# Optimization experiments

Hardware: AMD Instinct MI355X
Metric: run time of the kernel (lower is better)

The kernel has to match this reference:

```python
import jax, jax.numpy as jnp
import numpy as np

NEG_SLOPE = 0.2  # PyG GATConv default negative_slope


def gat_conv(x, edge_index, W, att_src, att_dst, b, num_nodes):
    """PyG-style GATConv: lin -> edge attention (LeakyReLU) -> segment softmax
    over destination nodes -> scatter-add aggregation. Self-loops added
    (PyG default add_self_loops=True). Heads concatenated."""
    H, C = att_src.shape
    h = (x @ W).reshape(num_nodes, H, C)            # [N, H, C]
    # add self loops
    loops = jnp.arange(num_nodes, dtype=edge_index.dtype)
    src = jnp.concatenate([edge_index[0], loops])   # [E+N]
    dst = jnp.concatenate([edge_index[1], loops])
    a_src = jnp.einsum('nhc,hc->nh', h, att_src)    # [N, H]
    a_dst = jnp.einsum('nhc,hc->nh', h, att_dst)
    alpha = a_src[src] + a_dst[dst]                 # [E+N, H]
    alpha = jnp.where(alpha > 0, alpha, NEG_SLOPE * alpha)  # LeakyReLU
    # numerically stable segment softmax over destination nodes
    amax = jax.lax.stop_gradient(
        jax.ops.segment_max(alpha, dst, num_segments=num_nodes))
    e = jnp.exp(alpha - amax[dst])
    denom = jax.ops.segment_sum(e, dst, num_segments=num_nodes)
    w = e / denom[dst]                              # [E+N, H]
    msg = h[src] * w[:, :, None]                    # [E+N, H, C]
    out = jax.ops.segment_sum(msg, dst, num_segments=num_nodes)  # [N, H, C]
    return out.reshape(num_nodes, H * C) + b


def setup_inputs() -> dict:
    key = jax.random.key(0)
    ks = jax.random.split(key, 12)
    N1, N2, E1, E2 = 50000, 10000, 800000, 160000
    IN, OUT, H = 256, 32, 4
    s = 0.1
    return {
        'x1': jax.random.normal(ks[0], (N1, IN), dtype=jnp.float32),
        'edge_index1': jax.random.randint(ks[1], (2, E1), 0, N1, dtype=jnp.int64),
        'x2': jax.random.normal(ks[2], (N2, IN), dtype=jnp.float32),
        'edge_index2': jax.random.randint(ks[3], (2, E2), 0, N2, dtype=jnp.int64),
        'group_assignment': jax.random.randint(ks[4], (N1,), 0, N2, dtype=jnp.int64),
        'W1': jax.random.normal(ks[5], (IN, H * OUT), dtype=jnp.float32) * s,
        'att_src1': jax.random.normal(ks[6], (H, OUT), dtype=jnp.float32) * s,
        'att_dst1': jax.random.normal(ks[7], (H, OUT), dtype=jnp.float32) * s,
        'b1': jnp.zeros((H * OUT,), dtype=jnp.float32),
        'W2': jax.random.normal(ks[8], (IN, H * OUT), dtype=jnp.float32) * s,
        'att_src2': jax.random.normal(ks[9], (H, OUT), dtype=jnp.float32) * s,
        'att_dst2': jax.random.normal(ks[10], (H, OUT), dtype=jnp.float32) * s,
        'b2': jnp.zeros((H * OUT,), dtype=jnp.float32),
    }


def reference(x1, edge_index1, x2, edge_index2, group_assignment,
              W1, att_src1, att_dst1, b1, W2, att_src2, att_dst2, b2):
    x1_out = gat_conv(x1, edge_index1, W1, att_src1, att_dst1, b1, x1.shape[0])
    x2_out = gat_conv(x2, edge_index2, W2, att_src2, att_dst2, b2, x2.shape[0])
    x1_combined = x1_out + x2_out[group_assignment]
    return (x1_combined, x2_out)
```

## Files before the change

### kernel.cpp

```cpp
#include <hip/hip_runtime.h>
#include <hip/hip_bf16.h>
#include <string.h>

#define IN_DIM 256
#define HC 128
#define HH 4
#define NEG_SLOPE 0.2f
#define BKT 64
#define NBMAX 1024
#define CAPB 2048

typedef __attribute__((ext_vector_type(8))) short bf16x8;
typedef __attribute__((ext_vector_type(4))) float f32x4;

__device__ __forceinline__ unsigned short f2b(float f) {
    __hip_bfloat16 h = __float2bfloat16(f);
    unsigned short u;
    memcpy(&u, &h, 2);
    return u;
}
__device__ __forceinline__ unsigned int pk2(float a, float b) {
    float2 t; t.x = a; t.y = b;
    __hip_bfloat162 p = __float22bfloat162_rn(t);
    unsigned int u;
    memcpy(&u, &p, 4);
    return u;
}
__device__ __forceinline__ bf16x8 cvt8(const float4 lo, const float4 hi) {
    union { unsigned int u[4]; bf16x8 v; } r;
    r.u[0] = pk2(lo.x, lo.y); r.u[1] = pk2(lo.z, lo.w);
    r.u[2] = pk2(hi.x, hi.y); r.u[3] = pk2(hi.z, hi.w);
    return r.v;
}
__device__ __forceinline__ float b2f(unsigned short u) {
    return __uint_as_float(((unsigned int)u) << 16);
}

__global__ void prep_kernel(const float* __restrict__ W1, const float* __restrict__ W2,
                            unsigned short* __restrict__ Wt1, unsigned short* __restrict__ Wt2) {
    const float* W = blockIdx.x ? W2 : W1;
    unsigned short* Wt = blockIdx.x ? Wt2 : Wt1;
    for (int idx = threadIdx.x; idx < HC * IN_DIM; idx += 256) {
        int c = idx >> 8, k = idx & 255;
        Wt[idx] = f2b(W[k * HC + c]);
    }
}

__device__ __forceinline__ void gemm_body(int blk, int tid,
                                          const float* __restrict__ x,
                                          const unsigned short* __restrict__ Wt,
                                          const float* __restrict__ attS,
                                          const float* __restrict__ attD,
                                          unsigned short* __restrict__ hb,
                                          float* __restrict__ asrc,
                                          float* __restrict__ adst, int N) {
    const int lane = tid & 63;
    const int wid = tid >> 6;
    const int lr = lane & 15, lg = lane >> 4;
    const int r0 = blk * 128 + wid * 32;
    int ra0 = r0 + lr;      if (ra0 > N - 1) ra0 = N - 1;
    int ra1 = r0 + 16 + lr; if (ra1 > N - 1) ra1 = N - 1;
    const float* A0 = x + (size_t)ra0 * IN_DIM + lg * 8;
    const float* A1 = x + (size_t)ra1 * IN_DIM + lg * 8;
    const unsigned short* B0 = Wt + (size_t)lr * IN_DIM + lg * 8;

    f32x4 acc[2][8];
#pragma unroll
    for (int h = 0; h < 2; ++h)
#pragma unroll
        for (int t = 0; t < 8; ++t) acc[h][t] = (f32x4){0.f, 0.f, 0.f, 0.f};

#pragma unroll
    for (int k0 = 0; k0 < IN_DIM; k0 += 32) {
        float4 a0l = *(const float4*)(A0 + k0);
        float4 a0h = *(const float4*)(A0 + k0 + 4);
        float4 a1l = *(const float4*)(A1 + k0);
        float4 a1h = *(const float4*)(A1 + k0 + 4);
        bf16x8 a0 = cvt8(a0l, a0h);
        bf16x8 a1 = cvt8(a1l, a1h);
#pragma unroll
        for (int t = 0; t < 8; ++t) {
            bf16x8 b = *(const bf16x8*)(B0 + t * 16 * IN_DIM + k0);
            acc[0][t] = __builtin_amdgcn_mfma_f32_16x16x32_bf16(a0, b, acc[0][t], 0, 0, 0);
            acc[1][t] = __builtin_amdgcn_mfma_f32_16x16x32_bf16(a1, b, acc[1][t], 0, 0, 0);
        }
    }

    float attS_r[8], attD_r[8];
#pragma unroll
    for (int t = 0; t < 8; ++t) {
        attS_r[t] = attS[t * 16 + lr];
        attD_r[t] = attD[t * 16 + lr];
    }

#pragma unroll
    for (int half = 0; half < 2; ++half) {
#pragma unroll
        for (int i = 0; i < 4; ++i) {
            int row = r0 + half * 16 + 4 * lg + i;
            float s[4] = {0.f, 0.f, 0.f, 0.f}, dd[4] = {0.f, 0.f, 0.f, 0.f};
#pragma unroll
            for (int t = 0; t < 8; ++t) {
                float c = acc[half][t][i];
                s[t >> 1] += c * attS_r[t];
                dd[t >> 1] += c * attD_r[t];
            }
#pragma unroll
            for (int m = 1; m < 16; m <<= 1) {
#pragma unroll
                for (int h = 0; h < 4; ++h) {
                    s[h] += __shfl_xor(s[h], m);
                    dd[h] += __shfl_xor(dd[h], m);
                }
            }
            if (row < N) {
#pragma unroll
                for (int t = 0; t < 8; ++t)
                    hb[(size_t)row * HC + t * 16 + lr] = f2b(acc[half][t][i]);
                if (lr == 0) {
#pragma unroll
                    for (int h = 0; h < 4; ++h) {
                        asrc[row * HH + h] = s[h];
                        adst[row * HH + h] = dd[h];
                    }
                }
            }
        }
    }
}

__launch_bounds__(256)
__global__ void mega_kernel(const float* __restrict__ x1,
                            const unsigned short* __restrict__ Wt1,
                            const float* __restrict__ attS1, const float* __restrict__ attD1,
                            unsigned short* __restrict__ hb1,
                            float* __restrict__ asrc1, float* __restrict__ adst1, int N1,
                            const float* __restrict__ x2,
                            const unsigned short* __restrict__ Wt2,
                            const float* __restrict__ attS2, const float* __restrict__ attD2,
                            unsigned short* __restrict__ hb2,
                            float* __restrict__ asrc2, float* __restrict__ adst2, int N2,
                            int G1) {
    const int b = blockIdx.x;
    const int tid = threadIdx.x;
    if (b < G1) gemm_body(b, tid, x1, Wt1, attS1, attD1, hb1, asrc1, adst1, N1);
    else        gemm_body(b - G1, tid, x2, Wt2, attS2, attD2, hb2, asrc2, adst2, N2);
}

__launch_bounds__(512)
__global__ void pass2_kernel(const int* __restrict__ ei1, int E1, int S1,
                             const int* __restrict__ ei2, int E2, int S2,
                             int nb1, int nbtot,
                             int* __restrict__ gcursor, int* __restrict__ rec) {
    __shared__ int hcnt[NBMAX];
    __shared__ int hoff[NBMAX];
    const int tid = threadIdx.x;
    for (int t = tid; t < NBMAX; t += 512) hcnt[t] = 0;
    __syncthreads();
    const int ebase = blockIdx.x * 4096;
    int myb[8], lrank[8], myrec[8];
#pragma unroll
    for (int k = 0; k < 8; ++k) {
        int i = ebase + tid + k * 512;
        int bkt = -1, src = 0, dstl = 0;
        if (i < S1) {
            int s, d;
            if (i < E1) { s = ei1[i]; d = ei1[E1 + i]; } else { s = d = i - E1; }
            bkt = d >> 6; src = s; dstl = d & 63;
        } else if (i < S1 + S2) {
            int q = i - S1, s, d;
            if (q < E2) { s = ei2[q]; d = ei2[E2 + q]; } else { s = d = q - E2; }
            bkt = nb1 + (d >> 6); src = s; dstl = d & 63;
        }
        myb[k] = bkt;
        myrec[k] = src | (dstl << 26);
        lrank[k] = (bkt >= 0) ? atomicAdd(&hcnt[bkt], 1) : 0;
    }
    __syncthreads();
    for (int t = tid; t < nbtot; t += 512)
        if (hcnt[t]) hoff[t] = atomicAdd(&gcursor[t], hcnt[t]);
    __syncthreads();
#pragma unroll
    for (int k = 0; k < 8; ++k) {
        int bkt = myb[k];
        if (bkt >= 0) {
            int pos = hoff[bkt] + lrank[k];
            if (pos < CAPB) rec[(size_t)bkt * CAPB + pos] = myrec[k];
        }
    }
}

__launch_bounds__(512)
__global__ void pass3_kernel(const int* __restrict__ rec, const int* __restrict__ gcursor,
                             int boff,
                             const unsigned short* __restrict__ hp,
                             const float* __restrict__ asrc, const float* __restrict__ adst,
                             const float* __restrict__ bias,
                             const int* __restrict__ ga,
                             const float* __restrict__ other,
                             float* __restrict__ out, int N) {
    __shared__ int srec[CAPB + 16];
    __shared__ int ncnt[BKT];
    __shared__ int nsc[BKT];
    __shared__ int ncur[BKT];
    __shared__ float adl[BKT * HH];
    const int tid = threadIdx.x;
    const int B = boff + blockIdx.x;
    const int n0 = blockIdx.x * BKT;
    int mycnt = gcursor[B];
    if (mycnt > CAPB) mycnt = CAPB;
    const int base = B * CAPB;

    for (int t = tid; t < BKT * HH; t += 512) {
        int node = n0 + (t >> 2);
        adl[t] = (node < N) ? adst[node * HH + (t & 3)] : 0.f;
    }
    if (tid < BKT) { ncnt[tid] = 0; ncur[tid] = 0; }
    __syncthreads();
    for (int t = tid; t < mycnt; t += 512) {
        int r = rec[base + t];
        atomicAdd(&ncnt[(r >> 26) & 63], 1);
    }
    __syncthreads();
    if (tid < 64) {
        int v = ncnt[tid];
#pragma unroll
        for (int off = 1; off < 64; off <<= 1) {
            int u = __shfl_up(v, off);
            if (tid >= off) v += u;
        }
        nsc[tid] = v;
    }
    if (tid < 16) srec[mycnt + tid] = 0;
    __syncthreads();
    for (int t = tid; t < mycnt; t += 512) {
        int r = rec[base + t];
        int dl = (r >> 26) & 63;
        int pos = nsc[dl] - ncnt[dl] + atomicAdd(&ncur[dl], 1);
        srec[pos] = r;
    }
    __syncthreads();

    const int slot = tid >> 5;
    const int j = tid & 31;
    const int head = j >> 3;
    const unsigned short* hbj = hp + 4 * j;

#pragma unroll
    for (int nl = 0; nl < 4; ++nl) {
        const int nloc = slot + (nl << 4);
        const int len = ncnt[nloc];
        float4 acc = {0.f, 0.f, 0.f, 0.f};
        float ws = 0.f;
        if (len > 0) {
            const int s0 = nsc[nloc] - len;
            const float adv = adl[nloc * HH + head];
            int rC[4], rN[4];
            float aC[4];
            ushort4 hC[4];
#pragma unroll
            for (int k = 0; k < 4; ++k) rC[k] = srec[s0 + k];
#pragma unroll
            for (int k = 0; k < 4; ++k) {
                int s = rC[k] & 0x3FFFFFF;
                aC[k] = asrc[s * HH + head];
                hC[k] = *(const ushort4*)(hbj + (size_t)s * HC);
            }
#pragma unroll
            for (int k = 0; k < 4; ++k) rN[k] = srec[s0 + 4 + k];
            for (int e = 0; e < len; e += 4) {
#pragma unroll
                for (int k = 0; k < 4; ++k) {
                    float alpha = aC[k] + adv;
                    alpha = alpha > 0.f ? alpha : NEG_SLOPE * alpha;
                    float w = (e + k < len) ? __expf(alpha) : 0.f;
                    acc.x += w * b2f(hC[k].x);
                    acc.y += w * b2f(hC[k].y);
                    acc.z += w * b2f(hC[k].z);
                    acc.w += w * b2f(hC[k].w);
                    ws += w;
                }
#pragma unroll
                for (int k = 0; k < 4; ++k) rC[k] = rN[k];
#pragma unroll
                for (int k = 0; k < 4; ++k) {
                    int s = rC[k] & 0x3FFFFFF;
                    aC[k] = asrc[s * HH + head];
                    hC[k] = *(const ushort4*)(hbj + (size_t)s * HC);
                }
#pragma unroll
                for (int k = 0; k < 4; ++k) rN[k] = srec[s0 + e + 8 + k];
            }
        }
        int node = n0 + nloc;
        if (node < N) {
            float inv = 1.f / ws;
            const float4 bb = *(const float4*)(bias + 4 * j);
            float4 o = {acc.x * inv + bb.x, acc.y * inv + bb.y,
                        acc.z * inv + bb.z, acc.w * inv + bb.w};
            if (ga) {
                const float4 ov = *(const float4*)(other + (size_t)ga[node] * HC + 4 * j);
                o.x += ov.x; o.y += ov.y; o.z += ov.z; o.w += ov.w;
            }
            *(float4*)(out + (size_t)node * HC + 4 * j) = o;
        }
    }
}

extern "C" void kernel_launch(void* const* d_in, const int* in_sizes, int n_in,
                              void* d_out, int out_size, void* d_ws, size_t ws_size,
                              hipStream_t stream) {
    const float* x1  = (const float*)d_in[0];
    const int*   ei1 = (const int*)d_in[1];
    const float* x2  = (const float*)d_in[2];
    const int*   ei2 = (const int*)d_in[3];
    const int*   ga  = (const int*)d_in[4];
    const float* W1    = (const float*)d_in[5];
    const float* attS1 = (const float*)d_in[6];
    const float* attD1 = (const float*)d_in[7];
    const float* b1    = (const float*)d_in[8];
    const float* W2    = (const float*)d_in[9];
    const float* attS2 = (const float*)d_in[10];
    const float* attD2 = (const float*)d_in[11];
    const float* b2    = (const float*)d_in[12];

    const int N1 = in_sizes[0] / IN_DIM;
    const int E1 = in_sizes[1] / 2;
    const int N2 = in_sizes[2] / IN_DIM;
    const int E2 = in_sizes[3] / 2;
    const int S1 = E1 + N1, S2 = E2 + N2;
    const int nb1 = (N1 + BKT - 1) / BKT;
    const int nb2 = (N2 + BKT - 1) / BKT;
    const int nbtot = nb1 + nb2;

    char* p = (char*)d_ws;
    auto alloc = [&](size_t bytes) {
        char* r = p; p += (bytes + 511) & ~(size_t)511; return r;
    };
    unsigned short* hb1 = (unsigned short*)alloc((size_t)N1 * HC * 2);
    unsigned short* hb2 = (unsigned short*)alloc((size_t)N2 * HC * 2);
    unsigned short* Wt1 = (unsigned short*)alloc((size_t)IN_DIM * HC * 2);
    unsigned short* Wt2 = (unsigned short*)alloc((size_t)IN_DIM * HC * 2);
    float* asrc1 = (float*)alloc((size_t)N1 * HH * 4);
    float* adst1 = (float*)alloc((size_t)N1 * HH * 4);
    float* asrc2 = (float*)alloc((size_t)N2 * HH * 4);
    float* adst2 = (float*)alloc((size_t)N2 * HH * 4);
    int* gcursor = (int*)alloc(NBMAX * 4);
    int* rec     = (int*)alloc((size_t)nbtot * CAPB * 4);

    float* out1 = (float*)d_out;
    float* out2 = (float*)d_out + (size_t)N1 * HC;

    (void)hipMemsetAsync(gcursor, 0, NBMAX * 4, stream);

    prep_kernel<<<2, 256, 0, stream>>>(W1, W2, Wt1, Wt2);

    const int G1 = (N1 + 127) / 128, G2 = (N2 + 127) / 128;
    mega_kernel<<<G1 + G2, 256, 0, stream>>>(
        x1, Wt1, attS1, attD1, hb1, asrc1, adst1, N1,
        x2, Wt2, attS2, attD2, hb2, asrc2, adst2, N2, G1);

    const int GP = (S1 + S2 + 4095) / 4096;
    pass2_kernel<<<GP, 512, 0, stream>>>(ei1, E1, S1, ei2, E2, S2,
                                         nb1, nbtot, gcursor, rec);

    pass3_kernel<<<nb2, 512, 0, stream>>>(rec, gcursor, nb1, hb2, asrc2, adst2,
                                          b2, nullptr, nullptr, out2, N2);
    pass3_kernel<<<nb1, 512, 0, stream>>>(rec, gcursor, 0, hb1, asrc1, adst1,
                                          b1, ga, out2, out1, N1);
}
```

Before: 130.2 us.

## Store h head-major and precompute bf16 edge weights in LDS for aggregation

The GEMM now writes projected features in a head-major layout ([H][N][32]), so each head's gather touches a 64-byte row. The aggregation kernel precomputes the exp(LeakyReLU) attention weights once per edge into a shared bf16 array, then processes one head at a time. Within each head, four edges are handled in parallel across lane groups, with a shuffle reduction at the end. This aims to cut redundant asrc loads and exp work and to shorten gathered rows, but it adds an extra LDS pass, rounds the weights to bf16, and runs four serial head loops per node.

```diff
diff --git a/kernel.cpp b/kernel.cpp
--- a/kernel.cpp
+++ b/kernel.cpp
@@ -51,7 +51,7 @@
                                           const unsigned short* __restrict__ Wt,
                                           const float* __restrict__ attS,
                                           const float* __restrict__ attD,
-                                          unsigned short* __restrict__ hb,
+                                          unsigned short* __restrict__ hq,
                                           float* __restrict__ asrc,
                                           float* __restrict__ adst, int N) {
     const int lane = tid & 63;
@@ -116,7 +116,8 @@
             if (row < N) {
 #pragma unroll
                 for (int t = 0; t < 8; ++t)
-                    hb[(size_t)row * HC + t * 16 + lr] = f2b(acc[half][t][i]);
+                    hq[((size_t)(t >> 1) * N + row) * 32 + (t & 1) * 16 + lr] =
+                        f2b(acc[half][t][i]);
                 if (lr == 0) {
 #pragma unroll
                     for (int h = 0; h < 4; ++h) {
@@ -133,18 +134,18 @@
 __global__ void mega_kernel(const float* __restrict__ x1,
                             const unsigned short* __restrict__ Wt1,
                             const float* __restrict__ attS1, const float* __restrict__ attD1,
-                            unsigned short* __restrict__ hb1,
+                            unsigned short* __restrict__ hq1,
                             float* __restrict__ asrc1, float* __restrict__ adst1, int N1,
                             const float* __restrict__ x2,
                             const unsigned short* __restrict__ Wt2,
                             const float* __restrict__ attS2, const float* __restrict__ attD2,
-                            unsigned short* __restrict__ hb2,
+                            unsigned short* __restrict__ hq2,
                             float* __restrict__ asrc2, float* __restrict__ adst2, int N2,
                             int G1) {
     const int b = blockIdx.x;
     const int tid = threadIdx.x;
-    if (b < G1) gemm_body(b, tid, x1, Wt1, attS1, attD1, hb1, asrc1, adst1, N1);
-    else        gemm_body(b - G1, tid, x2, Wt2, attS2, attD2, hb2, asrc2, adst2, N2);
+    if (b < G1) gemm_body(b, tid, x1, Wt1, attS1, attD1, hq1, asrc1, adst1, N1);
+    else        gemm_body(b - G1, tid, x2, Wt2, attS2, attD2, hq2, asrc2, adst2, N2);
 }
 
 __launch_bounds__(512)
@@ -193,13 +194,14 @@
 __launch_bounds__(512)
 __global__ void pass3_kernel(const int* __restrict__ rec, const int* __restrict__ gcursor,
                              int boff,
-                             const unsigned short* __restrict__ hp,
+                             const unsigned short* __restrict__ hq,
                              const float* __restrict__ asrc, const float* __restrict__ adst,
                              const float* __restrict__ bias,
                              const int* __restrict__ ga,
                              const float* __restrict__ other,
                              float* __restrict__ out, int N) {
     __shared__ int srec[CAPB + 16];
+    __shared__ unsigned short wrec[(CAPB + 16) * HH];
     __shared__ int ncnt[BKT];
     __shared__ int nsc[BKT];
     __shared__ int ncur[BKT];
@@ -217,10 +219,8 @@
     }
     if (tid < BKT) { ncnt[tid] = 0; ncur[tid] = 0; }
     __syncthreads();
-    for (int t = tid; t < mycnt; t += 512) {
-        int r = rec[base + t];
-        atomicAdd(&ncnt[(r >> 26) & 63], 1);
-    }
+    for (int t = tid; t < mycnt; t += 512)
+        atomicAdd(&ncnt[(rec[base + t] >> 26) & 63], 1);
     __syncthreads();
     if (tid < 64) {
         int v = ncnt[tid];
@@ -231,7 +231,11 @@
         }
         nsc[tid] = v;
     }
-    if (tid < 16) srec[mycnt + tid] = 0;
+    if (tid < 16) {
+        srec[mycnt + tid] = 0;
+#pragma unroll
+        for (int h = 0; h < HH; ++h) wrec[(mycnt + tid) * HH + h] = 0;
+    }
     __syncthreads();
     for (int t = tid; t < mycnt; t += 512) {
         int r = rec[base + t];
@@ -240,69 +244,77 @@
         srec[pos] = r;
     }
     __syncthreads();
+    for (int t = tid; t < mycnt; t += 512) {
+        int r = srec[t];
+        int s = r & 0x3FFFFFF;
+        int dl = (r >> 26) & 63;
+        const float4 a = *(const float4*)(asrc + (size_t)s * HH);
+        float al[4] = {a.x + adl[dl * HH + 0], a.y + adl[dl * HH + 1],
+                       a.z + adl[dl * HH + 2], a.w + adl[dl * HH + 3]};
+#pragma unroll
+        for (int h = 0; h < HH; ++h) {
+            float v = al[h];
+            v = v > 0.f ? v : NEG_SLOPE * v;
+            wrec[t * HH + h] = f2b(__expf(v));
+        }
+    }
+    __syncthreads();
 
     const int slot = tid >> 5;
     const int j = tid & 31;
-    const int head = j >> 3;
-    const unsigned short* hbj = hp + 4 * j;
+    const int g = j >> 3;
+    const int cj = j & 7;
 
 #pragma unroll
     for (int nl = 0; nl < 4; ++nl) {
         const int nloc = slot + (nl << 4);
         const int len = ncnt[nloc];
-        float4 acc = {0.f, 0.f, 0.f, 0.f};
-        float ws = 0.f;
-        if (len > 0) {
-            const int s0 = nsc[nloc] - len;
-            const float adv = adl[nloc * HH + head];
-            int rC[4], rN[4];
-            float aC[4];
-            ushort4 hC[4];
-#pragma unroll
-            for (int k = 0; k < 4; ++k) rC[k] = srec[s0 + k];
-#pragma unroll
-            for (int k = 0; k < 4; ++k) {
-                int s = rC[k] & 0x3FFFFFF;
-                aC[k] = asrc[s * HH + head];
-                hC[k] = *(const ushort4*)(hbj + (size_t)s * HC);
-            }
-#pragma unroll
-            for (int k = 0; k < 4; ++k) rN[k] = srec[s0 + 4 + k];
+        const int s0 = nsc[nloc] - len;
+        const int node = n0 + nloc;
+        int gnode = 0;
+        if (ga && node < N) gnode = ga[node];
+#pragma unroll
+        for (int h = 0; h < HH; ++h) {
+            const unsigned short* hqh = hq + (size_t)h * N * 32 + cj * 4;
+            float4 acc = {0.f, 0.f, 0.f, 0.f};
+            float ws = 0.f;
+            int idx = s0 + g;
+            float w = (g < len) ? b2f(wrec[idx * HH + h]) : 0.f;
+            int s = srec[idx] & 0x3FFFFFF;
+            ushort4 hv = *(const ushort4*)(hqh + (size_t)s * 32);
             for (int e = 0; e < len; e += 4) {
-#pragma unroll
-                for (int k = 0; k < 4; ++k) {
-                    float alpha = aC[k] + adv;
-                    alpha = alpha > 0.f ? alpha : NEG_SLOPE * alpha;
-                    float w = (e + k < len) ? __expf(alpha) : 0.f;
-                    acc.x += w * b2f(hC[k].x);
-                    acc.y += w * b2f(hC[k].y);
-                    acc.z += w * b2f(hC[k].z);
-                    acc.w += w * b2f(hC[k].w);
-                    ws += w;
+                float wc = w;
+                ushort4 hc = hv;
+                int nidx = idx + 4;
+                w = (e + 4 + g < len) ? b2f(wrec[nidx * HH + h]) : 0.f;
+                int ns = srec[nidx] & 0x3FFFFFF;
+                hv = *(const ushort4*)(hqh + (size_t)ns * 32);
+                idx = nidx;
+                acc.x += wc * b2f(hc.x);
+                acc.y += wc * b2f(hc.y);
+                acc.z += wc * b2f(hc.z);
+                acc.w += wc * b2f(hc.w);
+                ws += wc;
+            }
+#pragma unroll
+            for (int m = 8; m <= 16; m <<= 1) {
+                acc.x += __shfl_xor(acc.x, m);
+                acc.y += __shfl_xor(acc.y, m);
+                acc.z += __shfl_xor(acc.z, m);
+                acc.w += __shfl_xor(acc.w, m);
+                ws += __shfl_xor(ws, m);
+            }
+            if (g == 0 && node < N) {
+                float inv = 1.f / ws;
+                const float4 bb = *(const float4*)(bias + h * 32 + cj * 4);
+                float4 o = {acc.x * inv + bb.x, acc.y * inv + bb.y,
+                            acc.z * inv + bb.z, acc.w * inv + bb.w};
+                if (ga) {
+                    const float4 ov = *(const float4*)(other + (size_t)gnode * HC + h * 32 + cj * 4);
+                    o.x += ov.x; o.y += ov.y; o.z += ov.z; o.w += ov.w;
                 }
-#pragma unroll
-                for (int k = 0; k < 4; ++k) rC[k] = rN[k];
-#pragma unroll
-                for (int k = 0; k < 4; ++k) {
-                    int s = rC[k] & 0x3FFFFFF;
-                    aC[k] = asrc[s * HH + head];
-                    hC[k] = *(const ushort4*)(hbj + (size_t)s * HC);
-                }
-#pragma unroll
-                for (int k = 0; k < 4; ++k) rN[k] = srec[s0 + e + 8 + k];
-            }
-        }
-        int node = n0 + nloc;
-        if (node < N) {
-            float inv = 1.f / ws;
-            const float4 bb = *(const float4*)(bias + 4 * j);
-            float4 o = {acc.x * inv + bb.x, acc.y * inv + bb.y,
-                        acc.z * inv + bb.z, acc.w * inv + bb.w};
-            if (ga) {
-                const float4 ov = *(const float4*)(other + (size_t)ga[node] * HC + 4 * j);
-                o.x += ov.x; o.y += ov.y; o.z += ov.z; o.w += ov.w;
-            }
-            *(float4*)(out + (size_t)node * HC + 4 * j) = o;
+                *(float4*)(out + (size_t)node * HC + h * 32 + cj * 4) = o;
+            }
         }
     }
 }
@@ -337,8 +349,8 @@
     auto alloc = [&](size_t bytes) {
         char* r = p; p += (bytes + 511) & ~(size_t)511; return r;
     };
-    unsigned short* hb1 = (unsigned short*)alloc((size_t)N1 * HC * 2);
-    unsigned short* hb2 = (unsigned short*)alloc((size_t)N2 * HC * 2);
+    unsigned short* hq1 = (unsigned short*)alloc((size_t)N1 * HC * 2);
+    unsigned short* hq2 = (unsigned short*)alloc((size_t)N2 * HC * 2);
     unsigned short* Wt1 = (unsigned short*)alloc((size_t)IN_DIM * HC * 2);
     unsigned short* Wt2 = (unsigned short*)alloc((size_t)IN_DIM * HC * 2);
     float* asrc1 = (float*)alloc((size_t)N1 * HH * 4);
@@ -357,15 +369,15 @@
 
     const int G1 = (N1 + 127) / 128, G2 = (N2 + 127) / 128;
     mega_kernel<<<G1 + G2, 256, 0, stream>>>(
-        x1, Wt1, attS1, attD1, hb1, asrc1, adst1, N1,
-        x2, Wt2, attS2, attD2, hb2, asrc2, adst2, N2, G1);
+        x1, Wt1, attS1, attD1, hq1, asrc1, adst1, N1,
+        x2, Wt2, attS2, attD2, hq2, asrc2, adst2, N2, G1);
 
     const int GP = (S1 + S2 + 4095) / 4096;
     pass2_kernel<<<GP, 512, 0, stream>>>(ei1, E1, S1, ei2, E2, S2,
                                          nb1, nbtot, gcursor, rec);
 
-    pass3_kernel<<<nb2, 512, 0, stream>>>(rec, gcursor, nb1, hb2, asrc2, adst2,
+    pass3_kernel<<<nb2, 512, 0, stream>>>(rec, gcursor, nb1, hq2, asrc2, adst2,
                                           b2, nullptr, nullptr, out2, N2);
-    pass3_kernel<<<nb1, 512, 0, stream>>>(rec, gcursor, 0, hb1, asrc1, adst1,
+    pass3_kernel<<<nb1, 512, 0, stream>>>(rec, gcursor, 0, hq1, asrc1, adst1,
                                           b1, ga, out2, out1, N1);
 }
```

Result: slower. 162.7 us (+25.0%).

## Merge both aggregation passes into one launch with a flag dependency; halve GEMM tile

Applied to the files above, without the earlier changes.

The two pass3 launches (graph 2 then graph 1) become one grid. Graph-1 blocks do their aggregation first and only wait on a global atomic counter, set by the graph-2 blocks, before reading out2 for the group-assignment add. This removes a kernel boundary and lets the two graphs overlap, at the cost of a spin-wait that relies on graph-2 blocks being scheduled first. The GEMM tile also shrinks from 128 to 64 rows per block, giving more blocks and fewer accumulators per thread.

```diff
diff --git a/kernel.cpp b/kernel.cpp
--- a/kernel.cpp
+++ b/kernel.cpp
@@ -57,32 +57,24 @@
     const int lane = tid & 63;
     const int wid = tid >> 6;
     const int lr = lane & 15, lg = lane >> 4;
-    const int r0 = blk * 128 + wid * 32;
-    int ra0 = r0 + lr;      if (ra0 > N - 1) ra0 = N - 1;
-    int ra1 = r0 + 16 + lr; if (ra1 > N - 1) ra1 = N - 1;
-    const float* A0 = x + (size_t)ra0 * IN_DIM + lg * 8;
-    const float* A1 = x + (size_t)ra1 * IN_DIM + lg * 8;
+    const int r0 = blk * 64 + wid * 16;
+    int ra = r0 + lr; if (ra > N - 1) ra = N - 1;
+    const float* A = x + (size_t)ra * IN_DIM + lg * 8;
     const unsigned short* B0 = Wt + (size_t)lr * IN_DIM + lg * 8;
 
-    f32x4 acc[2][8];
-#pragma unroll
-    for (int h = 0; h < 2; ++h)
-#pragma unroll
-        for (int t = 0; t < 8; ++t) acc[h][t] = (f32x4){0.f, 0.f, 0.f, 0.f};
+    f32x4 acc[8];
+#pragma unroll
+    for (int t = 0; t < 8; ++t) acc[t] = (f32x4){0.f, 0.f, 0.f, 0.f};
 
 #pragma unroll
     for (int k0 = 0; k0 < IN_DIM; k0 += 32) {
-        float4 a0l = *(const float4*)(A0 + k0);
-        float4 a0h = *(const float4*)(A0 + k0 + 4);
-        float4 a1l = *(const float4*)(A1 + k0);
-        float4 a1h = *(const float4*)(A1 + k0 + 4);
-        bf16x8 a0 = cvt8(a0l, a0h);
-        bf16x8 a1 = cvt8(a1l, a1h);
+        float4 al = *(const float4*)(A + k0);
+        float4 ah = *(const float4*)(A + k0 + 4);
+        bf16x8 a = cvt8(al, ah);
 #pragma unroll
         for (int t = 0; t < 8; ++t) {
             bf16x8 b = *(const bf16x8*)(B0 + t * 16 * IN_DIM + k0);
-            acc[0][t] = __builtin_amdgcn_mfma_f32_16x16x32_bf16(a0, b, acc[0][t], 0, 0, 0);
-            acc[1][t] = __builtin_amdgcn_mfma_f32_16x16x32_bf16(a1, b, acc[1][t], 0, 0, 0);
+            acc[t] = __builtin_amdgcn_mfma_f32_16x16x32_bf16(a, b, acc[t], 0, 0, 0);
         }
     }
 
@@ -94,35 +86,32 @@
     }
 
 #pragma unroll
-    for (int half = 0; half < 2; ++half) {
-#pragma unroll
-        for (int i = 0; i < 4; ++i) {
-            int row = r0 + half * 16 + 4 * lg + i;
-            float s[4] = {0.f, 0.f, 0.f, 0.f}, dd[4] = {0.f, 0.f, 0.f, 0.f};
-#pragma unroll
-            for (int t = 0; t < 8; ++t) {
-                float c = acc[half][t][i];
-                s[t >> 1] += c * attS_r[t];
-                dd[t >> 1] += c * attD_r[t];
+    for (int i = 0; i < 4; ++i) {
+        int row = r0 + 4 * lg + i;
+        float s[4] = {0.f, 0.f, 0.f, 0.f}, dd[4] = {0.f, 0.f, 0.f, 0.f};
+#pragma unroll
+        for (int t = 0; t < 8; ++t) {
+            float c = acc[t][i];
+            s[t >> 1] += c * attS_r[t];
+            dd[t >> 1] += c * attD_r[t];
+        }
+#pragma unroll
+        for (int m = 1; m < 16; m <<= 1) {
+#pragma unroll
+            for (int h = 0; h < 4; ++h) {
+                s[h] += __shfl_xor(s[h], m);
+                dd[h] += __shfl_xor(dd[h], m);
             }
-#pragma unroll
-            for (int m = 1; m < 16; m <<= 1) {
+        }
+        if (row < N) {
+#pragma unroll
+            for (int t = 0; t < 8; ++t)
+                hb[(size_t)row * HC + t * 16 + lr] = f2b(acc[t][i]);
+            if (lr == 0) {
 #pragma unroll
                 for (int h = 0; h < 4; ++h) {
-                    s[h] += __shfl_xor(s[h], m);
-                    dd[h] += __shfl_xor(dd[h], m);
-                }
-            }
-            if (row < N) {
-#pragma unroll
-                for (int t = 0; t < 8; ++t)
-                    hb[(size_t)row * HC + t * 16 + lr] = f2b(acc[half][t][i]);
-                if (lr == 0) {
-#pragma unroll
-                    for (int h = 0; h < 4; ++h) {
-                        asrc[row * HH + h] = s[h];
-                        adst[row * HH + h] = dd[h];
-                    }
+                    asrc[row * HH + h] = s[h];
+                    adst[row * HH + h] = dd[h];
                 }
             }
         }
@@ -191,22 +180,38 @@
 }
 
 __launch_bounds__(512)
-__global__ void pass3_kernel(const int* __restrict__ rec, const int* __restrict__ gcursor,
-                             int boff,
-                             const unsigned short* __restrict__ hp,
-                             const float* __restrict__ asrc, const float* __restrict__ adst,
-                             const float* __restrict__ bias,
+__global__ void pass3_kernel(const int* __restrict__ rec, int* __restrict__ gcursor,
+                             int nb1, int nb2,
+                             const unsigned short* __restrict__ hb1,
+                             const float* __restrict__ asrc1, const float* __restrict__ adst1,
+                             const float* __restrict__ b1, int N1,
+                             const unsigned short* __restrict__ hb2,
+                             const float* __restrict__ asrc2, const float* __restrict__ adst2,
+                             const float* __restrict__ b2, int N2,
                              const int* __restrict__ ga,
-                             const float* __restrict__ other,
-                             float* __restrict__ out, int N) {
+                             float* __restrict__ out1, float* __restrict__ out2) {
     __shared__ int srec[CAPB + 16];
     __shared__ int ncnt[BKT];
     __shared__ int nsc[BKT];
     __shared__ int ncur[BKT];
     __shared__ float adl[BKT * HH];
     const int tid = threadIdx.x;
-    const int B = boff + blockIdx.x;
-    const int n0 = blockIdx.x * BKT;
+
+    const bool isG2 = (int)blockIdx.x < nb2;
+    int B, n0, N;
+    const unsigned short* hp;
+    const float *asrc, *adst, *bias;
+    float* out;
+    if (isG2) {
+        B = nb1 + blockIdx.x; n0 = blockIdx.x * BKT;
+        hp = hb2; asrc = asrc2; adst = adst2; bias = b2; out = out2; N = N2;
+    } else {
+        int g = blockIdx.x - nb2;
+        B = g; n0 = g * BKT;
+        hp = hb1; asrc = asrc1; adst = adst1; bias = b1; out = out1; N = N1;
+    }
+    int* flag = &gcursor[NBMAX - 1];
+
     int mycnt = gcursor[B];
     if (mycnt > CAPB) mycnt = CAPB;
     const int base = B * CAPB;
@@ -217,10 +222,8 @@
     }
     if (tid < BKT) { ncnt[tid] = 0; ncur[tid] = 0; }
     __syncthreads();
-    for (int t = tid; t < mycnt; t += 512) {
-        int r = rec[base + t];
-        atomicAdd(&ncnt[(r >> 26) & 63], 1);
-    }
+    for (int t = tid; t < mycnt; t += 512)
+        atomicAdd(&ncnt[(rec[base + t] >> 26) & 63], 1);
     __syncthreads();
     if (tid < 64) {
         int v = ncnt[tid];
@@ -246,6 +249,8 @@
     const int head = j >> 3;
     const unsigned short* hbj = hp + 4 * j;
 
+    float4 acc4[4];
+    float ws4[4];
 #pragma unroll
     for (int nl = 0; nl < 4; ++nl) {
         const int nloc = slot + (nl << 4);
@@ -292,18 +297,42 @@
                 for (int k = 0; k < 4; ++k) rN[k] = srec[s0 + e + 8 + k];
             }
         }
-        int node = n0 + nloc;
+        acc4[nl] = acc;
+        ws4[nl] = ws;
+    }
+
+    if (!isG2) {
+        if (tid == 0) {
+            while (__hip_atomic_load(flag, __ATOMIC_ACQUIRE,
+                                     __HIP_MEMORY_SCOPE_AGENT) < nb2)
+                __builtin_amdgcn_s_sleep(8);
+        }
+        __syncthreads();
+        __threadfence();
+    }
+
+#pragma unroll
+    for (int nl = 0; nl < 4; ++nl) {
+        int node = n0 + slot + (nl << 4);
         if (node < N) {
-            float inv = 1.f / ws;
+            float inv = 1.f / ws4[nl];
             const float4 bb = *(const float4*)(bias + 4 * j);
-            float4 o = {acc.x * inv + bb.x, acc.y * inv + bb.y,
-                        acc.z * inv + bb.z, acc.w * inv + bb.w};
-            if (ga) {
-                const float4 ov = *(const float4*)(other + (size_t)ga[node] * HC + 4 * j);
+            float4 o = {acc4[nl].x * inv + bb.x, acc4[nl].y * inv + bb.y,
+                        acc4[nl].z * inv + bb.z, acc4[nl].w * inv + bb.w};
+            if (!isG2) {
+                const float4 ov = *(const float4*)(out2 + (size_t)ga[node] * HC + 4 * j);
                 o.x += ov.x; o.y += ov.y; o.z += ov.z; o.w += ov.w;
             }
             *(float4*)(out + (size_t)node * HC + 4 * j) = o;
         }
+    }
+
+    if (isG2) {
+        __threadfence();
+        __syncthreads();
+        if (tid == 0)
+            __hip_atomic_fetch_add(flag, 1, __ATOMIC_RELEASE,
+                                   __HIP_MEMORY_SCOPE_AGENT);
     }
 }
 
@@ -355,7 +384,7 @@
 
     prep_kernel<<<2, 256, 0, stream>>>(W1, W2, Wt1, Wt2);
 
-    const int G1 = (N1 + 127) / 128, G2 = (N2 + 127) / 128;
+    const int G1 = (N1 + 63) / 64, G2 = (N2 + 63) / 64;
     mega_kernel<<<G1 + G2, 256, 0, stream>>>(
         x1, Wt1, attS1, attD1, hb1, asrc1, adst1, N1,
         x2, Wt2, attS2, attD2, hb2, asrc2, adst2, N2, G1);
@@ -364,8 +393,9 @@
     pass2_kernel<<<GP, 512, 0, stream>>>(ei1, E1, S1, ei2, E2, S2,
                                          nb1, nbtot, gcursor, rec);
 
-    pass3_kernel<<<nb2, 512, 0, stream>>>(rec, gcursor, nb1, hb2, asrc2, adst2,
-                                          b2, nullptr, nullptr, out2, N2);
-    pass3_kernel<<<nb1, 512, 0, stream>>>(rec, gcursor, 0, hb1, asrc1, adst1,
-                                          b1, ga, out2, out1, N1);
-}
+    pass3_kernel<<<nb2 + nb1, 512, 0, stream>>>(
+        rec, gcursor, nb1, nb2,
+        hb1, asrc1, adst1, b1, N1,
+        hb2, asrc2, adst2, b2, N2,
+        ga, out1, out2);
+}
```

Result: slower. 364.4 us (+179.9%).

## Fuse edge bucketing into GEMM launch and halve GEMM rows per block

Applied to the files above, without the earlier changes.

The edge-bucketing pass is folded into the same launch as the projection GEMM, with the first GP blocks doing bucketing and the rest doing GEMM, so the two independent phases can run concurrently and one launch is removed. The GEMM block now covers 64 rows (16 per wave) instead of 128, which doubles the block count and reduces accumulator registers. Bucketing now uses 256 threads with 16 edges each and packs bucket and local rank into one register. The trade-off is less reuse of the B loads per wave, and a shared-memory histogram is now allocated in GEMM blocks too, which may reduce occupancy.

```diff
diff --git a/kernel.cpp b/kernel.cpp
--- a/kernel.cpp
+++ b/kernel.cpp
@@ -57,32 +57,24 @@
     const int lane = tid & 63;
     const int wid = tid >> 6;
     const int lr = lane & 15, lg = lane >> 4;
-    const int r0 = blk * 128 + wid * 32;
-    int ra0 = r0 + lr;      if (ra0 > N - 1) ra0 = N - 1;
-    int ra1 = r0 + 16 + lr; if (ra1 > N - 1) ra1 = N - 1;
-    const float* A0 = x + (size_t)ra0 * IN_DIM + lg * 8;
-    const float* A1 = x + (size_t)ra1 * IN_DIM + lg * 8;
+    const int r0 = blk * 64 + wid * 16;
+    int ra = r0 + lr; if (ra > N - 1) ra = N - 1;
+    const float* A = x + (size_t)ra * IN_DIM + lg * 8;
     const unsigned short* B0 = Wt + (size_t)lr * IN_DIM + lg * 8;
 
-    f32x4 acc[2][8];
-#pragma unroll
-    for (int h = 0; h < 2; ++h)
-#pragma unroll
-        for (int t = 0; t < 8; ++t) acc[h][t] = (f32x4){0.f, 0.f, 0.f, 0.f};
+    f32x4 acc[8];
+#pragma unroll
+    for (int t = 0; t < 8; ++t) acc[t] = (f32x4){0.f, 0.f, 0.f, 0.f};
 
 #pragma unroll
     for (int k0 = 0; k0 < IN_DIM; k0 += 32) {
-        float4 a0l = *(const float4*)(A0 + k0);
-        float4 a0h = *(const float4*)(A0 + k0 + 4);
-        float4 a1l = *(const float4*)(A1 + k0);
-        float4 a1h = *(const float4*)(A1 + k0 + 4);
-        bf16x8 a0 = cvt8(a0l, a0h);
-        bf16x8 a1 = cvt8(a1l, a1h);
+        float4 al = *(const float4*)(A + k0);
+        float4 ah = *(const float4*)(A + k0 + 4);
+        bf16x8 a = cvt8(al, ah);
 #pragma unroll
         for (int t = 0; t < 8; ++t) {
             bf16x8 b = *(const bf16x8*)(B0 + t * 16 * IN_DIM + k0);
-            acc[0][t] = __builtin_amdgcn_mfma_f32_16x16x32_bf16(a0, b, acc[0][t], 0, 0, 0);
-            acc[1][t] = __builtin_amdgcn_mfma_f32_16x16x32_bf16(a1, b, acc[1][t], 0, 0, 0);
+            acc[t] = __builtin_amdgcn_mfma_f32_16x16x32_bf16(a, b, acc[t], 0, 0, 0);
         }
     }
 
@@ -94,37 +86,75 @@
     }
 
 #pragma unroll
-    for (int half = 0; half < 2; ++half) {
-#pragma unroll
-        for (int i = 0; i < 4; ++i) {
-            int row = r0 + half * 16 + 4 * lg + i;
-            float s[4] = {0.f, 0.f, 0.f, 0.f}, dd[4] = {0.f, 0.f, 0.f, 0.f};
-#pragma unroll
-            for (int t = 0; t < 8; ++t) {
-                float c = acc[half][t][i];
-                s[t >> 1] += c * attS_r[t];
-                dd[t >> 1] += c * attD_r[t];
-            }
-#pragma unroll
-            for (int m = 1; m < 16; m <<= 1) {
+    for (int i = 0; i < 4; ++i) {
+        int row = r0 + 4 * lg + i;
+        float s[4] = {0.f, 0.f, 0.f, 0.f}, dd[4] = {0.f, 0.f, 0.f, 0.f};
+#pragma unroll
+        for (int t = 0; t < 8; ++t) {
+            float c = acc[t][i];
+            s[t >> 1] += c * attS_r[t];
+            dd[t >> 1] += c * attD_r[t];
+        }
+#pragma unroll
+        for (int m = 1; m < 16; m <<= 1) {
+#pragma unroll
+            for (int h = 0; h < 4; ++h) {
+                s[h] += __shfl_xor(s[h], m);
+                dd[h] += __shfl_xor(dd[h], m);
+            }
+        }
+        if (row < N) {
+#pragma unroll
+            for (int t = 0; t < 8; ++t)
+                hb[(size_t)row * HC + t * 16 + lr] = f2b(acc[t][i]);
+            if (lr == 0) {
 #pragma unroll
                 for (int h = 0; h < 4; ++h) {
-                    s[h] += __shfl_xor(s[h], m);
-                    dd[h] += __shfl_xor(dd[h], m);
+                    asrc[row * HH + h] = s[h];
+                    adst[row * HH + h] = dd[h];
                 }
             }
-            if (row < N) {
-#pragma unroll
-                for (int t = 0; t < 8; ++t)
-                    hb[(size_t)row * HC + t * 16 + lr] = f2b(acc[half][t][i]);
-                if (lr == 0) {
-#pragma unroll
-                    for (int h = 0; h < 4; ++h) {
-                        asrc[row * HH + h] = s[h];
-                        adst[row * HH + h] = dd[h];
-                    }
-                }
-            }
+        }
+    }
+}
+
+__device__ __forceinline__ void pass2_body(int blk, int tid, int* hcnt, int* hoff,
+                                           const int* __restrict__ ei1, int E1, int S1,
+                                           const int* __restrict__ ei2, int E2, int S2,
+                                           int nb1, int nbtot,
+                                           int* __restrict__ gcursor,
+                                           int* __restrict__ rec) {
+    for (int t = tid; t < NBMAX; t += 256) hcnt[t] = 0;
+    __syncthreads();
+    const int ebase = blk * 4096;
+    int mypk[16], myrec[16];
+#pragma unroll
+    for (int k = 0; k < 16; ++k) {
+        int i = ebase + tid + k * 256;
+        int bkt = -1, src = 0, dstl = 0;
+        if (i < S1) {
+            int s, d;
+            if (i < E1) { s = ei1[i]; d = ei1[E1 + i]; } else { s = d = i - E1; }
+            bkt = d >> 6; src = s; dstl = d & 63;
+        } else if (i < S1 + S2) {
+            int q = i - S1, s, d;
+            if (q < E2) { s = ei2[q]; d = ei2[E2 + q]; } else { s = d = q - E2; }
+            bkt = nb1 + (d >> 6); src = s; dstl = d & 63;
+        }
+        myrec[k] = src | (dstl << 26);
+        int lrank = (bkt >= 0) ? atomicAdd(&hcnt[bkt], 1) : 0;
+        mypk[k] = (bkt >= 0) ? (bkt | (lrank << 16)) : -1;
+    }
+    __syncthreads();
+    for (int t = tid; t < nbtot; t += 256)
+        if (hcnt[t]) hoff[t] = atomicAdd(&gcursor[t], hcnt[t]);
+    __syncthreads();
+#pragma unroll
+    for (int k = 0; k < 16; ++k) {
+        if (mypk[k] >= 0) {
+            int bkt = mypk[k] & 0xFFFF;
+            int pos = hoff[bkt] + (mypk[k] >> 16);
+            if (pos < CAPB) rec[(size_t)bkt * CAPB + pos] = myrec[k];
         }
     }
 }
@@ -140,53 +170,22 @@
                             const float* __restrict__ attS2, const float* __restrict__ attD2,
                             unsigned short* __restrict__ hb2,
                             float* __restrict__ asrc2, float* __restrict__ adst2, int N2,
-                            int G1) {
+                            const int* __restrict__ ei1, int E1, int S1,
+                            const int* __restrict__ ei2, int E2, int S2,
+                            int nb1, int nbtot,
+                            int* __restrict__ gcursor, int* __restrict__ rec,
+                            int GP, int G1) {
+    __shared__ int hcnt[NBMAX];
+    __shared__ int hoff[NBMAX];
     const int b = blockIdx.x;
     const int tid = threadIdx.x;
-    if (b < G1) gemm_body(b, tid, x1, Wt1, attS1, attD1, hb1, asrc1, adst1, N1);
-    else        gemm_body(b - G1, tid, x2, Wt2, attS2, attD2, hb2, asrc2, adst2, N2);
-}
-
-__launch_bounds__(512)
-__global__ void pass2_kernel(const int* __restrict__ ei1, int E1, int S1,
-                             const int* __restrict__ ei2, int E2, int S2,
-                             int nb1, int nbtot,
-                             int* __restrict__ gcursor, int* __restrict__ rec) {
-    __shared__ int hcnt[NBMAX];
-    __shared__ int hoff[NBMAX];
-    const int tid = threadIdx.x;
-    for (int t = tid; t < NBMAX; t += 512) hcnt[t] = 0;
-    __syncthreads();
-    const int ebase = blockIdx.x * 4096;
-    int myb[8], lrank[8], myrec[8];
-#pragma unroll
-    for (int k = 0; k < 8; ++k) {
-        int i = ebase + tid + k * 512;
-        int bkt = -1, src = 0, dstl = 0;
-        if (i < S1) {
-            int s, d;
-            if (i < E1) { s = ei1[i]; d = ei1[E1 + i]; } else { s = d = i - E1; }
-            bkt = d >> 6; src = s; dstl = d & 63;
-        } else if (i < S1 + S2) {
-            int q = i - S1, s, d;
-            if (q < E2) { s = ei2[q]; d = ei2[E2 + q]; } else { s = d = q - E2; }
-            bkt = nb1 + (d >> 6); src = s; dstl = d & 63;
-        }
-        myb[k] = bkt;
-        myrec[k] = src | (dstl << 26);
-        lrank[k] = (bkt >= 0) ? atomicAdd(&hcnt[bkt], 1) : 0;
-    }
-    __syncthreads();
-    for (int t = tid; t < nbtot; t += 512)
-        if (hcnt[t]) hoff[t] = atomicAdd(&gcursor[t], hcnt[t]);
-    __syncthreads();
-#pragma unroll
-    for (int k = 0; k < 8; ++k) {
-        int bkt = myb[k];
-        if (bkt >= 0) {
-            int pos = hoff[bkt] + lrank[k];
-            if (pos < CAPB) rec[(size_t)bkt * CAPB + pos] = myrec[k];
-        }
+    if (b < GP) {
+        pass2_body(b, tid, hcnt, hoff, ei1, E1, S1, ei2, E2, S2,
+                   nb1, nbtot, gcursor, rec);
+    } else if (b < GP + G1) {
+        gemm_body(b - GP, tid, x1, Wt1, attS1, attD1, hb1, asrc1, adst1, N1);
+    } else {
+        gemm_body(b - GP - G1, tid, x2, Wt2, attS2, attD2, hb2, asrc2, adst2, N2);
     }
 }
 
@@ -217,10 +216,8 @@
     }
     if (tid < BKT) { ncnt[tid] = 0; ncur[tid] = 0; }
     __syncthreads();
-    for (int t = tid; t < mycnt; t += 512) {
-        int r = rec[base + t];
-        atomicAdd(&ncnt[(r >> 26) & 63], 1);
-    }
+    for (int t = tid; t < mycnt; t += 512)
+        atomicAdd(&ncnt[(rec[base + t] >> 26) & 63], 1);
     __syncthreads();
     if (tid < 64) {
         int v = ncnt[tid];
@@ -355,14 +352,12 @@
 
     prep_kernel<<<2, 256, 0, stream>>>(W1, W2, Wt1, Wt2);
 
-    const int G1 = (N1 + 127) / 128, G2 = (N2 + 127) / 128;
-    mega_kernel<<<G1 + G2, 256, 0, stream>>>(
+    const int GP = (S1 + S2 + 4095) / 4096;
+    const int G1 = (N1 + 63) / 64, G2 = (N2 + 63) / 64;
+    mega_kernel<<<GP + G1 + G2, 256, 0, stream>>>(
         x1, Wt1, attS1, attD1, hb1, asrc1, adst1, N1,
-        x2, Wt2, attS2, attD2, hb2, asrc2, adst2, N2, G1);
-
-    const int GP = (S1 + S2 + 4095) / 4096;
-    pass2_kernel<<<GP, 512, 0, stream>>>(ei1, E1, S1, ei2, E2, S2,
-                                         nb1, nbtot, gcursor, rec);
+        x2, Wt2, attS2, attD2, hb2, asrc2, adst2, N2,
+        ei1, E1, S1, ei2, E2, S2, nb1, nbtot, gcursor, rec, GP, G1);
 
     pass3_kernel<<<nb2, 512, 0, stream>>>(rec, gcursor, nb1, hb2, asrc2, adst2,
                                           b2, nullptr, nullptr, out2, N2);
```

Result: slower. 139.3 us (+7.0%).
